# Kernel optimization log

Measured on AMD Instinct MI355X. Metric: run time of the kernel, lower is better.

The kernel has to match this reference:

```python
import jax, jax.numpy as jnp
import numpy as np

B, L, IDIM = 1, 1024, 2048
H, DK, DV, K = 16, 128, 128, 4
KEY_DIM = H * DK          # 2048
VAL_DIM = H * DV          # 2048
CONV_DIM = 2 * KEY_DIM + VAL_DIM  # 6144
EPS = 1e-6


def setup_inputs() -> dict:
    key = jax.random.key(0)
    ks = jax.random.split(key, 8)
    s = 0.02
    x = jax.random.normal(ks[0], (B, L, IDIM), jnp.float32)
    Wqkv = jax.random.normal(ks[1], (IDIM, CONV_DIM), jnp.float32) * s
    Wz = jax.random.normal(ks[2], (IDIM, VAL_DIM), jnp.float32) * s
    Wb = jax.random.normal(ks[3], (IDIM, H), jnp.float32) * s
    Wa = jax.random.normal(ks[4], (IDIM, H), jnp.float32) * s
    conv_w = jax.random.normal(ks[5], (CONV_DIM, 1, K), jnp.float32) * 0.2  # depthwise [O,I/g=1,K]
    A_log = jnp.log(jax.random.uniform(ks[6], (H,), jnp.float32, 0.1, 16.0))
    dt_bias = jnp.ones((H,), jnp.float32)
    norm_w = jnp.ones((DV,), jnp.float32)
    Wout = jax.random.normal(ks[7], (VAL_DIM, IDIM), jnp.float32) * s
    return dict(x=x, Wqkv=Wqkv, Wz=Wz, Wb=Wb, Wa=Wa, conv_w=conv_w,
                A_log=A_log, dt_bias=dt_bias, norm_w=norm_w, Wout=Wout)


def _l2norm(t):
    return t * jax.lax.rsqrt(jnp.sum(t * t, axis=-1, keepdims=True) + EPS)


def reference(x, Wqkv, Wz, Wb, Wa, conv_w, A_log, dt_bias, norm_w, Wout):
    b, l, _ = x.shape
    # fused QKV projection + causal depthwise conv + SiLU
    qkv = jnp.einsum('bld,dc->blc', x, Wqkv)                 # [B,L,CONV_DIM]
    qkv = jnp.transpose(qkv, (0, 2, 1))                      # [B,C,L]
    qkv = jax.lax.conv_general_dilated(
        qkv, conv_w, window_strides=(1,), padding=[(K - 1, 0)],
        dimension_numbers=('NCL', 'OIL', 'NCL'), feature_group_count=CONV_DIM)
    qkv = jax.nn.silu(jnp.transpose(qkv, (0, 2, 1)))         # [B,L,C]
    q, k, v = jnp.split(qkv, [KEY_DIM, 2 * KEY_DIM], axis=-1)

    z = jnp.einsum('bld,dv->blv', x, Wz)                     # [B,L,VAL_DIM]
    beta = jax.nn.sigmoid(jnp.einsum('bld,dh->blh', x, Wb))  # [B,L,H]
    A = -jnp.exp(A_log)                                      # [H]
    dt = jax.nn.softplus(jnp.einsum('bld,dh->blh', x, Wa) + dt_bias)
    g = dt * A                                               # [B,L,H] (negative)

    q = _l2norm(q.reshape(b, l, H, DK))
    k = _l2norm(k.reshape(b, l, H, DK))
    v = v.reshape(b, l, H, DV)
    scale = DK ** -0.5

    # time-major for scan: [L,B,H,...]
    qs = jnp.transpose(q, (1, 0, 2, 3)) * scale
    ks_ = jnp.transpose(k, (1, 0, 2, 3))
    vs = jnp.transpose(v, (1, 0, 2, 3))
    bs = jnp.transpose(beta, (1, 0, 2))
    gs = jnp.transpose(g, (1, 0, 2))

    M0 = jnp.zeros((b, H, DK, DV), jnp.float32)

    def step(M, inp):
        q_t, k_t, v_t, b_t, g_t = inp
        M = M * jnp.exp(g_t)[..., None, None]                    # decay
        Mk = jnp.einsum('bhd,bhdv->bhv', k_t, M)                 # readout of old mem
        M = M + jnp.einsum('bhd,bhv->bhdv', k_t, (v_t - Mk) * b_t[..., None])
        o_t = jnp.einsum('bhd,bhdv->bhv', q_t, M)
        return M, o_t

    _, out = jax.lax.scan(step, M0, (qs, ks_, vs, bs, gs))   # out: [L,B,H,DV]
    out = jnp.transpose(out, (1, 0, 2, 3))                   # [B,L,H,DV]

    # RMSNormGated: rms_norm(o) * weight * silu(z)
    zg = z.reshape(b, l, H, DV)
    rms = jax.lax.rsqrt(jnp.mean(out * out, axis=-1, keepdims=True) + EPS)
    out = (out * rms) * norm_w * jax.nn.silu(zg)

    out = out.reshape(b, l, VAL_DIM)
    return jnp.einsum('blv,vd->bld', out, Wout)
```

## Files before the change

### kernel.cpp

```cpp
#include <hip/hip_runtime.h>

typedef short bf16x8 __attribute__((ext_vector_type(8)));
typedef float f32x4 __attribute__((ext_vector_type(4)));
typedef float f32x2 __attribute__((ext_vector_type(2)));
typedef unsigned short u16;
typedef u16 u16x4 __attribute__((ext_vector_type(4)));

#define L_SEQ 1024
#define IDIM_ 2048
#define H_ 16
#define DK_ 128
#define DV_ 128
#define KEYD 2048
#define VALD 2048
#define CONVD 6144
#define QZD 8192
#define CH 16
#define NCH (L_SEQ / CH)
#define SCH 64
#define NSC (L_SEQ / SCH)

__device__ __forceinline__ u16 f2bf(float f) {
  union { float f; unsigned u; } v; v.f = f;
  unsigned r = v.u + 0x7FFF + ((v.u >> 16) & 1);
  return (u16)(r >> 16);
}

__device__ __forceinline__ float red16(float x) {
  union U { float f; int i; } a, t;
  a.f = x;
  t.i = __builtin_amdgcn_update_dpp(0, a.i, 0xB1, 0xF, 0xF, true); a.f += t.f;
  t.i = __builtin_amdgcn_update_dpp(0, a.i, 0x4E, 0xF, 0xF, true); a.f += t.f;
  t.i = __builtin_amdgcn_update_dpp(0, a.i, 0x141, 0xF, 0xF, true); a.f += t.f;
  t.i = __builtin_amdgcn_update_dpp(0, a.i, 0x140, 0xF, 0xF, true); a.f += t.f;
  return a.f;
}

__device__ __forceinline__ void gl_lds16(const float* g, float* l) {
  __builtin_amdgcn_global_load_lds(
      (const __attribute__((address_space(1))) void*)g,
      (__attribute__((address_space(3))) void*)l, 16, 0, 0);
}
__device__ __forceinline__ void gl_lds4(const float* g, float* l) {
  __builtin_amdgcn_global_load_lds(
      (const __attribute__((address_space(1))) void*)g,
      (__attribute__((address_space(3))) void*)l, 4, 0, 0);
}

__global__ __launch_bounds__(256) void prepcast_kernel(const float* __restrict__ x,
                                                       const float* __restrict__ Wqkv,
                                                       const float* __restrict__ Wz,
                                                       const float* __restrict__ Wout,
                                                       u16* __restrict__ xb,
                                                       u16* __restrict__ WcatT,
                                                       u16* __restrict__ WoutT) {
  __shared__ float tile[32][33];
  const int bid = blockIdx.x;
  if (bid < 2048) {
    int i = (bid * 256 + threadIdx.x) * 4;
    f32x4 v = *(const f32x4*)&x[i];
    u16x4 o = { f2bf(v[0]), f2bf(v[1]), f2bf(v[2]), f2bf(v[3]) };
    *(u16x4*)&xb[i] = o;
    return;
  }
  const float* W; u16* WT; int R, C, bx, by;
  if (bid < 14336) {
    int t = bid - 2048;  bx = t % 192; by = t / 192;
    W = Wqkv; WT = WcatT; R = IDIM_; C = CONVD;
  } else if (bid < 18432) {
    int t = bid - 14336; bx = t & 63; by = t >> 6;
    W = Wz; WT = WcatT + (size_t)CONVD * IDIM_; R = IDIM_; C = VALD;
  } else {
    int t = bid - 18432; bx = t & 63; by = t >> 6;
    W = Wout; WT = WoutT; R = VALD; C = IDIM_;
  }
  int c0 = bx * 32, r0 = by * 32;
  int tx = threadIdx.x & 31, ty = threadIdx.x >> 5;
#pragma unroll
  for (int j = 0; j < 4; ++j)
    tile[ty + j * 8][tx] = W[(size_t)(r0 + ty + j * 8) * C + c0 + tx];
  __syncthreads();
#pragma unroll
  for (int j = 0; j < 4; ++j)
    WT[(size_t)(c0 + ty + j * 8) * R + r0 + tx] = f2bf(tile[tx][ty + j * 8]);
}

__global__ __launch_bounds__(256) void gemm_bt_kernel(const u16* __restrict__ A,
                                                      const u16* __restrict__ B,
                                                      float* __restrict__ C,
                                                      int M, int N, int K, int cxl) {
  __shared__ short As[128 * 72];
  __shared__ short Bs[128 * 72];
  const int tid = threadIdx.x;
  const int lane = tid & 63, wave = tid >> 6;
  const int wm = wave >> 1, wn = wave & 1;
  const int bid = blockIdx.x;
  const int xcd = bid & 7, bi = bid >> 3;
  const int bx = (xcd << cxl) + (bi & ((1 << cxl) - 1));
  const int by = bi >> cxl;
  const int m0 = by * 128, n0 = bx * 128;
  const int l15 = lane & 15, lhi = lane >> 4;

  f32x4 acc[4][4] = {};

  for (int k0 = 0; k0 < K; k0 += 64) {
    __syncthreads();
#pragma unroll
    for (int i = 0; i < 4; ++i) {
      int chunk = tid + i * 256;
      int row = chunk >> 3;
      int kc = (chunk & 7) * 8;
      *(bf16x8*)&As[row * 72 + kc] =
          *(const bf16x8*)&A[(size_t)(m0 + row) * K + k0 + kc];
      *(bf16x8*)&Bs[row * 72 + kc] =
          *(const bf16x8*)&B[(size_t)(n0 + row) * K + k0 + kc];
    }
    __syncthreads();
#pragma unroll
    for (int kk = 0; kk < 64; kk += 32) {
      const int koff = kk + lhi * 8;
      bf16x8 a[4], b[4];
#pragma unroll
      for (int m = 0; m < 4; ++m)
        a[m] = *(const bf16x8*)&As[(wm * 64 + m * 16 + l15) * 72 + koff];
#pragma unroll
      for (int n = 0; n < 4; ++n)
        b[n] = *(const bf16x8*)&Bs[(wn * 64 + n * 16 + l15) * 72 + koff];
#pragma unroll
      for (int m = 0; m < 4; ++m)
#pragma unroll
        for (int n = 0; n < 4; ++n)
          acc[m][n] = __builtin_amdgcn_mfma_f32_16x16x32_bf16(a[m], b[n], acc[m][n], 0, 0, 0);
    }
  }
#pragma unroll
  for (int m = 0; m < 4; ++m)
#pragma unroll
    for (int n = 0; n < 4; ++n)
#pragma unroll
      for (int j = 0; j < 4; ++j) {
        int row = m0 + wm * 64 + m * 16 + lhi * 4 + j;
        int col = n0 + wn * 64 + n * 16 + l15;
        C[(size_t)row * N + col] = acc[m][n][j];
      }
}

__global__ __launch_bounds__(256) void gemm_bt64_kernel(const u16* __restrict__ A,
                                                        const u16* __restrict__ B,
                                                        float* __restrict__ C,
                                                        int M, int N, int K, int cxl) {
  __shared__ short As[64 * 72];
  __shared__ short Bs[128 * 72];
  const int tid = threadIdx.x;
  const int lane = tid & 63, wave = tid >> 6;
  const int wm = wave >> 1, wn = wave & 1;
  const int bid = blockIdx.x;
  const int xcd = bid & 7, bi = bid >> 3;
  const int bx = (xcd << cxl) + (bi & ((1 << cxl) - 1));
  const int by = bi >> cxl;
  const int m0 = by * 64, n0 = bx * 128;
  const int l15 = lane & 15, lhi = lane >> 4;

  f32x4 acc[2][4] = {};

  for (int k0 = 0; k0 < K; k0 += 64) {
    __syncthreads();
#pragma unroll
    for (int i = 0; i < 2; ++i) {
      int chunk = tid + i * 256;
      int row = chunk >> 3;
      int kc = (chunk & 7) * 8;
      *(bf16x8*)&As[row * 72 + kc] =
          *(const bf16x8*)&A[(size_t)(m0 + row) * K + k0 + kc];
    }
#pragma unroll
    for (int i = 0; i < 4; ++i) {
      int chunk = tid + i * 256;
      int row = chunk >> 3;
      int kc = (chunk & 7) * 8;
      *(bf16x8*)&Bs[row * 72 + kc] =
          *(const bf16x8*)&B[(size_t)(n0 + row) * K + k0 + kc];
    }
    __syncthreads();
#pragma unroll
    for (int kk = 0; kk < 64; kk += 32) {
      const int koff = kk + lhi * 8;
      bf16x8 a[2], b[4];
#pragma unroll
      for (int m = 0; m < 2; ++m)
        a[m] = *(const bf16x8*)&As[(wm * 32 + m * 16 + l15) * 72 + koff];
#pragma unroll
      for (int n = 0; n < 4; ++n)
        b[n] = *(const bf16x8*)&Bs[(wn * 64 + n * 16 + l15) * 72 + koff];
#pragma unroll
      for (int m = 0; m < 2; ++m)
#pragma unroll
        for (int n = 0; n < 4; ++n)
          acc[m][n] = __builtin_amdgcn_mfma_f32_16x16x32_bf16(a[m], b[n], acc[m][n], 0, 0, 0);
    }
  }
#pragma unroll
  for (int m = 0; m < 2; ++m)
#pragma unroll
    for (int n = 0; n < 4; ++n)
#pragma unroll
      for (int j = 0; j < 4; ++j) {
        int row = m0 + wm * 32 + m * 16 + lhi * 4 + j;
        int col = n0 + wn * 64 + n * 16 + l15;
        C[(size_t)row * N + col] = acc[m][n][j];
      }
}

__global__ __launch_bounds__(128) void betag_kernel(const float* __restrict__ x,
                                                    const float* __restrict__ Wb,
                                                    const float* __restrict__ Wa,
                                                    const float* __restrict__ A_log,
                                                    const float* __restrict__ dt_bias,
                                                    float* __restrict__ btT,
                                                    float* __restrict__ egT,
                                                    float* __restrict__ gT) {
  int l = blockIdx.x;
  __shared__ float xs[IDIM_];
  __shared__ float redb[128], reda[128];
  for (int i = threadIdx.x; i < IDIM_; i += 128) xs[i] = x[(size_t)l * IDIM_ + i];
  __syncthreads();
  int h = threadIdx.x & 15, part = threadIdx.x >> 4;
  float sb = 0.f, sa = 0.f;
  int d0 = part * 256;
  for (int d = d0; d < d0 + 256; ++d) {
    float xv = xs[d];
    sb += xv * Wb[d * 16 + h];
    sa += xv * Wa[d * 16 + h];
  }
  redb[threadIdx.x] = sb;
  reda[threadIdx.x] = sa;
  __syncthreads();
  if (threadIdx.x < 16) {
    float b = 0.f, a = 0.f;
#pragma unroll
    for (int p = 0; p < 8; ++p) { b += redb[p * 16 + h]; a += reda[p * 16 + h]; }
    btT[h * L_SEQ + l] = 1.f / (1.f + expf(-b));
    float dtv = a + dt_bias[h];
    dtv = (dtv > 20.f) ? dtv : log1pf(expf(dtv));
    float g = -expf(A_log[h]) * dtv;
    egT[h * L_SEQ + l] = expf(g);
    gT[h * L_SEQ + l] = g;
  }
}

__global__ __launch_bounds__(256) void prep2_kernel(const float* __restrict__ qkvz,
                                                    const float* __restrict__ cw,
                                                    float* __restrict__ qn,
                                                    float* __restrict__ kn,
                                                    float* __restrict__ vT) {
  __shared__ float tile[32][33];
  const int bid = blockIdx.x;
  if (bid < 4096) {
    int wid = bid * 4 + (threadIdx.x >> 6);
    int lane = threadIdx.x & 63;
    int l = wid >> 4, h = wid & 15;
    const int cq = h * 128 + lane * 2;
    const int ck = KEYD + cq;
    const float* row0 = qkvz + (size_t)l * QZD;
    f32x4 wq0 = *(const f32x4*)&cw[cq * 4];
    f32x4 wq1 = *(const f32x4*)&cw[(cq + 1) * 4];
    f32x4 wk0 = *(const f32x4*)&cw[ck * 4];
    f32x4 wk1 = *(const f32x4*)&cw[(ck + 1) * 4];
    f32x2 xq = *(const f32x2*)&row0[cq];
    f32x2 xk = *(const f32x2*)&row0[ck];
    float q0 = xq[0] * wq0[3], q1 = xq[1] * wq1[3];
    float k0 = xk[0] * wk0[3], k1 = xk[1] * wk1[3];
    if (l >= 1) {
      f32x2 aq = *(const f32x2*)&row0[cq - QZD];
      f32x2 ak = *(const f32x2*)&row0[ck - QZD];
      q0 += aq[0] * wq0[2]; q1 += aq[1] * wq1[2];
      k0 += ak[0] * wk0[2]; k1 += ak[1] * wk1[2];
    }
    if (l >= 2) {
      f32x2 aq = *(const f32x2*)&row0[cq - 2 * QZD];
      f32x2 ak = *(const f32x2*)&row0[ck - 2 * QZD];
      q0 += aq[0] * wq0[1]; q1 += aq[1] * wq1[1];
      k0 += ak[0] * wk0[1]; k1 += ak[1] * wk1[1];
    }
    if (l >= 3) {
      f32x2 aq = *(const f32x2*)&row0[cq - 3 * QZD];
      f32x2 ak = *(const f32x2*)&row0[ck - 3 * QZD];
      q0 += aq[0] * wq0[0]; q1 += aq[1] * wq1[0];
      k0 += ak[0] * wk0[0]; k1 += ak[1] * wk1[0];
    }
    f32x2 qv = { q0 / (1.f + expf(-q0)), q1 / (1.f + expf(-q1)) };
    f32x2 kv = { k0 / (1.f + expf(-k0)), k1 / (1.f + expf(-k1)) };

    float ssq = qv[0] * qv[0] + qv[1] * qv[1];
    float ssk = kv[0] * kv[0] + kv[1] * kv[1];
#pragma unroll
    for (int s = 1; s < 64; s <<= 1) {
      ssq += __shfl_xor(ssq, s);
      ssk += __shfl_xor(ssk, s);
    }
    float scq = 0.08838834764831845f / sqrtf(ssq + 1e-6f);
    float sck = 1.f / sqrtf(ssk + 1e-6f);
    qv[0] *= scq; qv[1] *= scq;
    kv[0] *= sck; kv[1] *= sck;
    size_t base = ((size_t)h * L_SEQ + l) * 128 + lane * 2;
    *(f32x2*)&qn[base] = qv;
    *(f32x2*)&kn[base] = kv;
    return;
  }
  int t = bid - 4096;
  int c0 = (t & 63) * 32, l0 = (t >> 6) * 32;
  int tx = threadIdx.x & 31, ty = threadIdx.x >> 5;
  const int c = 2 * KEYD + c0 + tx;
  f32x4 w = *(const f32x4*)&cw[c * 4];
#pragma unroll
  for (int j = 0; j < 4; ++j) {
    int l = l0 + ty + j * 8;
    const float* p = qkvz + (size_t)l * QZD + c;
    float s = p[0] * w[3];
    if (l >= 1) s += p[-QZD] * w[2];
    if (l >= 2) s += p[-2 * QZD] * w[1];
    if (l >= 3) s += p[-3 * QZD] * w[0];
    tile[ty + j * 8][tx] = s / (1.f + expf(-s));
  }
  __syncthreads();
#pragma unroll
  for (int j = 0; j < 4; ++j)
    vT[(size_t)(c0 + ty + j * 8) * L_SEQ + l0 + tx] = tile[tx][ty + j * 8];
}

__global__ __launch_bounds__(256) void scan_kernel(const float* __restrict__ kn,
                                                   const float* __restrict__ vT,
                                                   const float* __restrict__ egT,
                                                   const float* __restrict__ btT,
                                                   float* __restrict__ Mb,
                                                   float* __restrict__ DbT) {
  __shared__ alignas(16) float ks[2][CH][128];
  __shared__ alignas(16) float vs[2][16][CH];
  __shared__ alignas(16) float ebc[2][2][CH];

  const int tid = threadIdx.x;
  const int wave = tid >> 6, lane = tid & 63;
  const int dk_sub = lane & 15;
  const int head = blockIdx.x & 15;
  const int dv0 = (blockIdx.x >> 4) * 16;
  const int col_local = tid >> 4;
  const int dv = dv0 + col_local;

  const float* kh = kn + (size_t)head * L_SEQ * 128;

  auto stage = [&](int chunk, int buf) {
    const int l0 = chunk * CH;
    const float* kg = kh + (size_t)l0 * 128;
#pragma unroll
    for (int i = 0; i < 2; ++i) {
      int seg = i * 4 + wave;
      int off = seg * 256 + lane * 4;
      gl_lds16(kg + off, &ks[buf][0][0] + seg * 256);
    }
    {
      int idx = wave * 64 + lane;
      gl_lds4(vT + (size_t)(head * 128 + dv0 + (idx >> 4)) * L_SEQ + l0 + (idx & 15),
              &vs[buf][0][0] + wave * 64);
    }
    if (wave == 0 && lane < 32) {
      const float* src = (lane < 16) ? (egT + head * L_SEQ + l0 + lane)
                                     : (btT + head * L_SEQ + l0 + (lane - 16));
      gl_lds4(src, &ebc[buf][0][0]);
    }
  };

  stage(0, 0);
  __syncthreads();

  f32x4 Mlo = {0.f, 0.f, 0.f, 0.f}, Mhi = {0.f, 0.f, 0.f, 0.f};
  const int dkb = dk_sub * 8;
  float* dcol = DbT + (size_t)(head * 128 + dv) * L_SEQ;

#pragma unroll 1
  for (int c = 0; c < NCH; ++c) {
    const int buf = c & 1;
    if (c + 1 < NCH) stage(c + 1, buf ^ 1);

    if ((c & 3) == 0) {
      int sc = c >> 2;
      float* mrow = Mb + (((size_t)sc * 16 + head) * 128 + dv) * 128 + dkb;
      *(f32x4*)mrow = Mlo;
      *(f32x4*)(mrow + 4) = Mhi;
    }

    f32x4 ev[4], bv[4], vv[4];
#pragma unroll
    for (int i = 0; i < 4; ++i) {
      ev[i] = *(const f32x4*)&ebc[buf][0][i * 4];
      bv[i] = *(const f32x4*)&ebc[buf][1][i * 4];
      vv[i] = *(const f32x4*)&vs[buf][col_local][i * 4];
    }
    f32x4 kr[4][2];
#pragma unroll
    for (int i = 0; i < 3; ++i) {
      kr[i][0] = *(const f32x4*)&ks[buf][i][dkb];
      kr[i][1] = *(const f32x4*)&ks[buf][i][dkb + 4];
    }

#pragma unroll
    for (int s = 0; s < CH; ++s) {
      if (s + 3 < CH) {
        kr[(s + 3) & 3][0] = *(const f32x4*)&ks[buf][s + 3][dkb];
        kr[(s + 3) & 3][1] = *(const f32x4*)&ks[buf][s + 3][dkb + 4];
      }
      const f32x4 k0 = kr[s & 3][0], k1 = kr[s & 3][1];
      const float e = ev[s >> 2][s & 3], b = bv[s >> 2][s & 3];
      const float v = vv[s >> 2][s & 3];

      float skm0 = k0[0] * Mlo[0], skm1 = k0[1] * Mlo[1];
      skm0 = fmaf(k0[2], Mlo[2], skm0); skm1 = fmaf(k0[3], Mlo[3], skm1);
      skm0 = fmaf(k1[0], Mhi[0], skm0); skm1 = fmaf(k1[1], Mhi[1], skm1);
      skm0 = fmaf(k1[2], Mhi[2], skm0); skm1 = fmaf(k1[3], Mhi[3], skm1);
      f32x4 emlo, emhi;
#pragma unroll
      for (int i = 0; i < 4; ++i) { emlo[i] = e * Mlo[i]; emhi[i] = e * Mhi[i]; }
      float skm = red16(skm0 + skm1);
      float dl = (v - e * skm) * b;
      if (dk_sub == 0) dcol[c * CH + s] = dl;
#pragma unroll
      for (int i = 0; i < 4; ++i) {
        Mlo[i] = fmaf(k0[i], dl, emlo[i]);
        Mhi[i] = fmaf(k1[i], dl, emhi[i]);
      }
    }
    __syncthreads();
  }
}

__global__ __launch_bounds__(256) void opass_kernel(const float* __restrict__ qn,
                                                    const float* __restrict__ kn,
                                                    const float* __restrict__ DbT,
                                                    const float* __restrict__ gT,
                                                    const float* __restrict__ Mb,
                                                    const float* __restrict__ qkvz,
                                                    const float* __restrict__ norm_w,
                                                    u16* __restrict__ gn) {
  __shared__ alignas(16) u16 qsb[64][136];
  __shared__ alignas(16) u16 bbuf[128][136];
  __shared__ alignas(16) u16 Asb[64][72];
  __shared__ float gsh[64], Gh[64];
  __shared__ float ssr[2][64];

  const int tid = threadIdx.x;
  const int lane = tid & 63, wave = tid >> 6;
  const int l15 = lane & 15, lhi = lane >> 4;
  const int h = blockIdx.x & 15, sc = blockIdx.x >> 4;
  const int l0 = sc * SCH;

  {
    int t = tid >> 2, c0 = (tid & 3) * 32;
    const float* qr = qn + ((size_t)h * L_SEQ + l0 + t) * 128 + c0;
    const float* kr = kn + ((size_t)h * L_SEQ + l0 + t) * 128 + c0;
#pragma unroll
    for (int j = 0; j < 8; ++j) {
      f32x4 vq = *(const f32x4*)&qr[j * 4];
      f32x4 vk = *(const f32x4*)&kr[j * 4];
      u16x4 oq = { f2bf(vq[0]), f2bf(vq[1]), f2bf(vq[2]), f2bf(vq[3]) };
      u16x4 ok = { f2bf(vk[0]), f2bf(vk[1]), f2bf(vk[2]), f2bf(vk[3]) };
      *(u16x4*)&qsb[t][c0 + j * 4] = oq;
      *(u16x4*)&bbuf[t][c0 + j * 4] = ok;
    }
  }
  if (tid < 64) gsh[tid] = gT[h * L_SEQ + l0 + tid];
  __syncthreads();
  if (tid < 64) {
    float a = 0.f;
    for (int u = 0; u <= tid; ++u) a += gsh[u];
    Gh[tid] = a;
  }
  __syncthreads();

  f32x4 acc1[2][2] = {};
  const int wm = wave >> 1, wn = wave & 1;
#pragma unroll
  for (int kk = 0; kk < 128; kk += 32) {
    const int koff = kk + lhi * 8;
    bf16x8 a[2], b[2];
#pragma unroll
    for (int m = 0; m < 2; ++m)
      a[m] = *(const bf16x8*)&qsb[wm * 32 + m * 16 + l15][koff];
#pragma unroll
    for (int n = 0; n < 2; ++n)
      b[n] = *(const bf16x8*)&bbuf[wn * 32 + n * 16 + l15][koff];
#pragma unroll
    for (int m = 0; m < 2; ++m)
#pragma unroll
      for (int n = 0; n < 2; ++n)
        acc1[m][n] = __builtin_amdgcn_mfma_f32_16x16x32_bf16(a[m], b[n], acc1[m][n], 0, 0, 0);
  }
#pragma unroll
  for (int m = 0; m < 2; ++m)
#pragma unroll
    for (int n = 0; n < 2; ++n)
#pragma unroll
      for (int j = 0; j < 4; ++j) {
        int t = wm * 32 + m * 16 + lhi * 4 + j;
        int s = wn * 32 + n * 16 + l15;
        float a = (s <= t) ? acc1[m][n][j] * expf(Gh[t] - Gh[s]) : 0.f;
        Asb[t][s] = f2bf(a);
      }
  __syncthreads();

  {
    int dv = tid >> 1, c0 = (tid & 1) * 64;
    const float* mr = Mb + (((size_t)sc * 16 + h) * 128 + dv) * 128 + c0;
#pragma unroll
    for (int j = 0; j < 16; ++j) {
      f32x4 v = *(const f32x4*)&mr[j * 4];
      u16x4 o = { f2bf(v[0]), f2bf(v[1]), f2bf(v[2]), f2bf(v[3]) };
      *(u16x4*)&bbuf[dv][c0 + j * 4] = o;
    }
  }
  __syncthreads();

  f32x4 acc[2][4] = {};
#pragma unroll
  for (int kk = 0; kk < 128; kk += 32) {
    const int koff = kk + lhi * 8;
    bf16x8 a[2], b[4];
#pragma unroll
    for (int m = 0; m < 2; ++m)
      a[m] = *(const bf16x8*)&qsb[wm * 32 + m * 16 + l15][koff];
#pragma unroll
    for (int n = 0; n < 4; ++n)
      b[n] = *(const bf16x8*)&bbuf[wn * 64 + n * 16 + l15][koff];
#pragma unroll
    for (int m = 0; m < 2; ++m)
#pragma unroll
      for (int n = 0; n < 4; ++n)
        acc[m][n] = __builtin_amdgcn_mfma_f32_16x16x32_bf16(a[m], b[n], acc[m][n], 0, 0, 0);
  }
#pragma unroll
  for (int m = 0; m < 2; ++m) {
#pragma unroll
    for (int j = 0; j < 4; ++j) {
      int t = wm * 32 + m * 16 + lhi * 4 + j;
      float sc1 = expf(Gh[t]);
#pragma unroll
      for (int n = 0; n < 4; ++n) acc[m][n][j] *= sc1;
    }
  }
  __syncthreads();

  {
    int dv = tid >> 1, c0 = (tid & 1) * 32;
    const float* dr = DbT + (size_t)(h * 128 + dv) * L_SEQ + l0 + c0;
#pragma unroll
    for (int j = 0; j < 8; ++j) {
      f32x4 v = *(const f32x4*)&dr[j * 4];
      u16x4 o = { f2bf(v[0]), f2bf(v[1]), f2bf(v[2]), f2bf(v[3]) };
      *(u16x4*)&bbuf[dv][c0 + j * 4] = o;
    }
  }
  __syncthreads();

#pragma unroll
  for (int kk = 0; kk < 64; kk += 32) {
    const int koff = kk + lhi * 8;
    bf16x8 a[2], b[4];
#pragma unroll
    for (int m = 0; m < 2; ++m)
      a[m] = *(const bf16x8*)&Asb[wm * 32 + m * 16 + l15][koff];
#pragma unroll
    for (int n = 0; n < 4; ++n)
      b[n] = *(const bf16x8*)&bbuf[wn * 64 + n * 16 + l15][koff];
#pragma unroll
    for (int m = 0; m < 2; ++m)
#pragma unroll
      for (int n = 0; n < 4; ++n)
        acc[m][n] = __builtin_amdgcn_mfma_f32_16x16x32_bf16(a[m], b[n], acc[m][n], 0, 0, 0);
  }

  float pr[2][4];
#pragma unroll
  for (int m = 0; m < 2; ++m)
#pragma unroll
    for (int j = 0; j < 4; ++j) {
      float p = 0.f;
#pragma unroll
      for (int n = 0; n < 4; ++n) p = fmaf(acc[m][n][j], acc[m][n][j], p);
      pr[m][j] = red16(p);
    }
  if (l15 == 0) {
#pragma unroll
    for (int m = 0; m < 2; ++m)
#pragma unroll
      for (int j = 0; j < 4; ++j)
        ssr[wn][wm * 32 + m * 16 + lhi * 4 + j] = pr[m][j];
  }
  __syncthreads();
#pragma unroll
  for (int m = 0; m < 2; ++m)
#pragma unroll
    for (int j = 0; j < 4; ++j) {
      int t = wm * 32 + m * 16 + lhi * 4 + j;
      float ss = ssr[0][t] + ssr[1][t];
      float r = 1.f / sqrtf(ss * (1.f / 128.f) + 1e-6f);
      const float* zp = qkvz + (size_t)(l0 + t) * QZD + CONVD + h * 128;
      u16* dst = gn + (size_t)(l0 + t) * VALD + h * 128;
#pragma unroll
      for (int n = 0; n < 4; ++n) {
        int dv = wn * 64 + n * 16 + l15;
        float z = zp[dv];
        float sil = z / (1.f + expf(-z));
        dst[dv] = f2bf(acc[m][n][j] * r * norm_w[dv] * sil);
      }
    }
}

extern "C" void kernel_launch(void* const* d_in, const int* in_sizes, int n_in,
                              void* d_out, int out_size, void* d_ws, size_t ws_size,
                              hipStream_t stream) {
  const float* x      = (const float*)d_in[0];
  const float* Wqkv   = (const float*)d_in[1];
  const float* Wz     = (const float*)d_in[2];
  const float* Wb     = (const float*)d_in[3];
  const float* Wa     = (const float*)d_in[4];
  const float* conv_w = (const float*)d_in[5];
  const float* A_log  = (const float*)d_in[6];
  const float* dt_bias= (const float*)d_in[7];
  const float* norm_w = (const float*)d_in[8];
  const float* Wout   = (const float*)d_in[9];
  float* out = (float*)d_out;

  char* ws = (char*)d_ws;
  size_t off = 0;
  auto alloc = [&](size_t bytes) {
    void* p = ws + off;
    off = (off + bytes + 255) & ~(size_t)255;
    return p;
  };
  u16* xb     = (u16*)alloc((size_t)L_SEQ * IDIM_ * 2);
  u16* WcatT  = (u16*)alloc((size_t)QZD * IDIM_ * 2);
  u16* WoutT  = (u16*)alloc((size_t)IDIM_ * VALD * 2);
  float* qkvz = (float*)alloc((size_t)L_SEQ * QZD * 4);
  float* qn   = (float*)alloc((size_t)H_ * L_SEQ * 128 * 4);
  float* kn   = (float*)alloc((size_t)H_ * L_SEQ * 128 * 4);
  float* vT   = (float*)alloc((size_t)H_ * 128 * L_SEQ * 4);
  float* btT  = (float*)alloc((size_t)L_SEQ * H_ * 4);
  float* egT  = (float*)alloc((size_t)L_SEQ * H_ * 4);
  float* gTb  = (float*)alloc((size_t)L_SEQ * H_ * 4);
  float* Mb   = (float*)alloc((size_t)NSC * H_ * 128 * 128 * 4);
  float* DbT  = (float*)alloc((size_t)H_ * 128 * L_SEQ * 4);
  u16* gn     = (u16*)alloc((size_t)L_SEQ * VALD * 2);

  prepcast_kernel<<<22528, 256, 0, stream>>>(x, Wqkv, Wz, Wout, xb, WcatT, WoutT);

  gemm_bt_kernel<<<512, 256, 0, stream>>>(xb, WcatT, qkvz, L_SEQ, QZD, IDIM_, 3);

  betag_kernel<<<L_SEQ, 128, 0, stream>>>(x, Wb, Wa, A_log, dt_bias, btT, egT, gTb);

  prep2_kernel<<<6144, 256, 0, stream>>>(qkvz, conv_w, qn, kn, vT);

  scan_kernel<<<H_ * (DV_ / 16), 256, 0, stream>>>(kn, vT, egT, btT, Mb, DbT);

  opass_kernel<<<NSC * H_, 256, 0, stream>>>(qn, kn, DbT, gTb, Mb, qkvz, norm_w, gn);

  gemm_bt64_kernel<<<256, 256, 0, stream>>>(gn, WoutT, out, L_SEQ, IDIM_, VALD, 1);
}
```

Before: 338.3 us.

## Fold beta/alpha projections into the main QKVZ GEMM as extra columns

Appends Wb and Wa (cast to bf16, zero-padded to a 128-column tile) to the concatenated weight matrix so the main GEMM also computes the beta and dt pre-activations. The separate fp32 betag kernel, which re-read x and did scalar dot products, is replaced by a small elementwise gate kernel that reads those columns. This removes a serial, poorly parallel kernel but adds one more column tile to the GEMM, computes the gates in bf16 precision, and drops the XCD-aware block remapping in favour of a plain 2D grid.

```diff
diff --git a/kernel.cpp b/kernel.cpp
--- a/kernel.cpp
+++ b/kernel.cpp
@@ -14,7 +14,8 @@
 #define KEYD 2048
 #define VALD 2048
 #define CONVD 6144
-#define QZD 8192
+#define QZD 8320
+#define GCOL 8192
 #define CH 16
 #define NCH (L_SEQ / CH)
 #define SCH 64
@@ -50,6 +51,8 @@
 __global__ __launch_bounds__(256) void prepcast_kernel(const float* __restrict__ x,
                                                        const float* __restrict__ Wqkv,
                                                        const float* __restrict__ Wz,
+                                                       const float* __restrict__ Wb,
+                                                       const float* __restrict__ Wa,
                                                        const float* __restrict__ Wout,
                                                        u16* __restrict__ xb,
                                                        u16* __restrict__ WcatT,
@@ -63,6 +66,25 @@
     *(u16x4*)&xb[i] = o;
     return;
   }
+  if (bid >= 22592) {
+    size_t off = (size_t)8224 * IDIM_ + (size_t)(bid - 22592) * 8192 + threadIdx.x * 32;
+    u16x4 z = {0, 0, 0, 0};
+#pragma unroll
+    for (int j = 0; j < 8; ++j) *(u16x4*)&WcatT[off + j * 4] = z;
+    return;
+  }
+  if (bid >= 22528) {
+    int by = bid - 22528;
+    int r = threadIdx.x >> 3, c8 = threadIdx.x & 7;
+    int row = by * 32 + r;
+#pragma unroll
+    for (int cc = 0; cc < 2; ++cc) {
+      int c = cc * 8 + c8;
+      WcatT[(size_t)(GCOL + c) * IDIM_ + row]      = f2bf(Wb[(size_t)row * 16 + c]);
+      WcatT[(size_t)(GCOL + 16 + c) * IDIM_ + row] = f2bf(Wa[(size_t)row * 16 + c]);
+    }
+    return;
+  }
   const float* W; u16* WT; int R, C, bx, by;
   if (bid < 14336) {
     int t = bid - 2048;  bx = t % 192; by = t / 192;
@@ -88,17 +110,13 @@
 __global__ __launch_bounds__(256) void gemm_bt_kernel(const u16* __restrict__ A,
                                                       const u16* __restrict__ B,
                                                       float* __restrict__ C,
-                                                      int M, int N, int K, int cxl) {
+                                                      int M, int N, int K) {
   __shared__ short As[128 * 72];
   __shared__ short Bs[128 * 72];
   const int tid = threadIdx.x;
   const int lane = tid & 63, wave = tid >> 6;
   const int wm = wave >> 1, wn = wave & 1;
-  const int bid = blockIdx.x;
-  const int xcd = bid & 7, bi = bid >> 3;
-  const int bx = (xcd << cxl) + (bi & ((1 << cxl) - 1));
-  const int by = bi >> cxl;
-  const int m0 = by * 128, n0 = bx * 128;
+  const int m0 = blockIdx.y * 128, n0 = blockIdx.x * 128;
   const int l15 = lane & 15, lhi = lane >> 4;
 
   f32x4 acc[4][4] = {};
@@ -211,41 +229,22 @@
       }
 }
 
-__global__ __launch_bounds__(128) void betag_kernel(const float* __restrict__ x,
-                                                    const float* __restrict__ Wb,
-                                                    const float* __restrict__ Wa,
-                                                    const float* __restrict__ A_log,
-                                                    const float* __restrict__ dt_bias,
-                                                    float* __restrict__ btT,
-                                                    float* __restrict__ egT,
-                                                    float* __restrict__ gT) {
-  int l = blockIdx.x;
-  __shared__ float xs[IDIM_];
-  __shared__ float redb[128], reda[128];
-  for (int i = threadIdx.x; i < IDIM_; i += 128) xs[i] = x[(size_t)l * IDIM_ + i];
-  __syncthreads();
-  int h = threadIdx.x & 15, part = threadIdx.x >> 4;
-  float sb = 0.f, sa = 0.f;
-  int d0 = part * 256;
-  for (int d = d0; d < d0 + 256; ++d) {
-    float xv = xs[d];
-    sb += xv * Wb[d * 16 + h];
-    sa += xv * Wa[d * 16 + h];
-  }
-  redb[threadIdx.x] = sb;
-  reda[threadIdx.x] = sa;
-  __syncthreads();
-  if (threadIdx.x < 16) {
-    float b = 0.f, a = 0.f;
-#pragma unroll
-    for (int p = 0; p < 8; ++p) { b += redb[p * 16 + h]; a += reda[p * 16 + h]; }
-    btT[h * L_SEQ + l] = 1.f / (1.f + expf(-b));
-    float dtv = a + dt_bias[h];
-    dtv = (dtv > 20.f) ? dtv : log1pf(expf(dtv));
-    float g = -expf(A_log[h]) * dtv;
-    egT[h * L_SEQ + l] = expf(g);
-    gT[h * L_SEQ + l] = g;
-  }
+__global__ __launch_bounds__(256) void gatelite_kernel(const float* __restrict__ qkvz,
+                                                       const float* __restrict__ A_log,
+                                                       const float* __restrict__ dt_bias,
+                                                       float* __restrict__ btT,
+                                                       float* __restrict__ egT,
+                                                       float* __restrict__ gT) {
+  int gid = blockIdx.x * 256 + threadIdx.x;
+  int l = gid >> 4, h = gid & 15;
+  const float* row = qkvz + (size_t)l * QZD + GCOL;
+  float b = row[h], a = row[16 + h];
+  btT[h * L_SEQ + l] = 1.f / (1.f + expf(-b));
+  float dtv = a + dt_bias[h];
+  dtv = (dtv > 20.f) ? dtv : log1pf(expf(dtv));
+  float g = -expf(A_log[h]) * dtv;
+  egT[h * L_SEQ + l] = expf(g);
+  gT[h * L_SEQ + l] = g;
 }
 
 __global__ __launch_bounds__(256) void prep2_kernel(const float* __restrict__ qkvz,
@@ -649,11 +648,11 @@
   float* DbT  = (float*)alloc((size_t)H_ * 128 * L_SEQ * 4);
   u16* gn     = (u16*)alloc((size_t)L_SEQ * VALD * 2);
 
-  prepcast_kernel<<<22528, 256, 0, stream>>>(x, Wqkv, Wz, Wout, xb, WcatT, WoutT);
-
-  gemm_bt_kernel<<<512, 256, 0, stream>>>(xb, WcatT, qkvz, L_SEQ, QZD, IDIM_, 3);
-
-  betag_kernel<<<L_SEQ, 128, 0, stream>>>(x, Wb, Wa, A_log, dt_bias, btT, egT, gTb);
+  prepcast_kernel<<<22616, 256, 0, stream>>>(x, Wqkv, Wz, Wb, Wa, Wout, xb, WcatT, WoutT);
+
+  gemm_bt_kernel<<<dim3(QZD / 128, L_SEQ / 128), 256, 0, stream>>>(xb, WcatT, qkvz, L_SEQ, QZD, IDIM_);
+
+  gatelite_kernel<<<64, 256, 0, stream>>>(qkvz, A_log, dt_bias, btT, egT, gTb);
 
   prep2_kernel<<<6144, 256, 0, stream>>>(qkvz, conv_w, qn, kn, vT);
 
```

After: 322.0 us, median of 2. -4.8%, faster.
